# Kernel tuning notes

Measured on AMD Instinct MI355X. Metric: run time of the kernel, lower is better.

## Reference

```python
import jax, jax.numpy as jnp
import numpy as np

N_NODES = 50000
N_EDGES = 800000
NUM_FEATURES = 128
HIDDEN = 128
NUM_GRAPHS = 500


def setup_inputs() -> dict:
    key = jax.random.key(0)
    ks = jax.random.split(key, 8)
    def lin_w(k, fan_in, fan_out):
        bound = 1.0 / np.sqrt(fan_in)
        return jax.random.uniform(k, (fan_in, fan_out), jnp.float32, -bound, bound)
    x = jax.random.normal(ks[0], (N_NODES, NUM_FEATURES), jnp.float32)
    W0 = lin_w(ks[1], NUM_FEATURES, HIDDEN)
    W1 = lin_w(ks[2], HIDDEN, HIDDEN)
    W2 = lin_w(ks[3], HIDDEN, HIDDEN)
    Wout = lin_w(ks[4], HIDDEN, 1)
    b0 = jnp.zeros((HIDDEN,), jnp.float32)
    b1 = jnp.zeros((HIDDEN,), jnp.float32)
    b2 = jnp.zeros((HIDDEN,), jnp.float32)
    bout = jnp.zeros((1,), jnp.float32)
    edge_index = jax.random.randint(ks[5], (2, N_EDGES), 0, N_NODES, jnp.int64)
    batch = jnp.sort(jax.random.randint(ks[6], (N_NODES,), 0, NUM_GRAPHS, jnp.int64))
    return {"x": x, "W0": W0, "b0": b0, "W1": W1, "b1": b1, "W2": W2,
            "b2": b2, "Wout": Wout, "bout": bout,
            "edge_index": edge_index, "batch": batch}


def _gcn_conv(x, W, b, row, col, norm, n_nodes):
    # GCNConv: out = D^{-1/2} (A + I) D^{-1/2} X W + b
    xw = x @ W                                  # [N, H] dense GEMM
    msg = xw[row] * norm[:, None]               # gather + scale  [E+N, H]
    out = jax.ops.segment_sum(msg, col, num_segments=n_nodes)  # scatter-add
    return out + b


def _gcn_norm(edge_index, n_nodes):
    # add self-loops, then symmetric degree normalization
    loops = jnp.arange(n_nodes, dtype=edge_index.dtype)
    row = jnp.concatenate([edge_index[0], loops])  # source (j)
    col = jnp.concatenate([edge_index[1], loops])  # target (i)
    deg = jax.ops.segment_sum(jnp.ones_like(col, dtype=jnp.float32), col,
                              num_segments=n_nodes)
    dinv = jnp.where(deg > 0, jax.lax.rsqrt(jnp.maximum(deg, 1.0)), 0.0)
    norm = dinv[row] * dinv[col]
    return row, col, norm


def reference(x, W0, b0, W1, b1, W2, b2, Wout, bout, edge_index, batch):
    n_nodes = x.shape[0]
    row, col, norm = _gcn_norm(edge_index, n_nodes)
    h = x
    for (W, b) in ((W0, b0), (W1, b1), (W2, b2)):
        h = _gcn_conv(h, W, b, row, col, norm, n_nodes)
        h = jax.nn.elu(h)
        # F.dropout(training=False) -> identity in eval mode
    # global_mean_pool over graph ids
    sums = jax.ops.segment_sum(h, batch, num_segments=NUM_GRAPHS)
    cnts = jax.ops.segment_sum(jnp.ones((n_nodes,), h.dtype), batch,
                               num_segments=NUM_GRAPHS)
    pooled = sums / jnp.maximum(cnts, 1.0)[:, None]   # [G, H]
    return pooled @ Wout + bout                       # [G, 1]
```

## Files before the change

kernel.cpp:

```cpp
#include <hip/hip_runtime.h>
#include <math.h>

#define NN 50000
#define NE 800000
#define HD 128
#define NG 500
#define CAP 48
#define GEMM_BLKS 782
#define FILL_BLKS 384
#define FRONT_GRID (GEMM_BLKS + FILL_BLKS)

__global__ __launch_bounds__(256) void k_front(const float* __restrict__ x,
                                               const float* __restrict__ W,
                                               const int* __restrict__ erow,
                                               const int* __restrict__ ecol,
                                               int* __restrict__ deg,
                                               unsigned short* __restrict__ rec,
                                               float* __restrict__ XW) {
    __shared__ float Hs[64][36];
    __shared__ float Ws[32][132];

    const int bid = blockIdx.x;
    const int tid = threadIdx.x;

    if (bid >= GEMM_BLKS) {
        for (int e = (bid - GEMM_BLKS) * 256 + tid; e < NE; e += FILL_BLKS * 256) {
            int r = erow[e];
            int c = ecol[e];
            int p = atomicAdd(&deg[c], 1);
            p = p < CAP - 1 ? p : CAP - 1;
            rec[c * CAP + p] = (unsigned short)r;
        }
        return;
    }

    const int base = bid * 64;
    const int tr = tid >> 4;
    const int tc = tid & 15;
    const int c0 = tc * 8;

    float acc[4][8];
#pragma unroll
    for (int i = 0; i < 4; ++i)
#pragma unroll
        for (int j = 0; j < 8; ++j) acc[i][j] = 0.f;

    for (int kc = 0; kc < 4; ++kc) {
        __syncthreads();
#pragma unroll
        for (int i = 0; i < 2; ++i) {
            int idx = i * 256 + tid;
            int r = idx >> 3;
            int c4 = idx & 7;
            int row = base + r;
            float4 v = make_float4(0.f, 0.f, 0.f, 0.f);
            if (row < NN) v = *(const float4*)(x + (size_t)row * HD + kc * 32 + c4 * 4);
            *(float4*)&Hs[r][c4 * 4] = v;
        }
#pragma unroll
        for (int i = 0; i < 4; ++i) {
            int idx = i * 256 + tid;
            int kr = idx >> 5;
            int c4 = idx & 31;
            float4 v = *(const float4*)(W + (size_t)(kc * 32 + kr) * HD + c4 * 4);
            *(float4*)&Ws[kr][c4 * 4] = v;
        }
        __syncthreads();
#pragma unroll
        for (int k4 = 0; k4 < 8; ++k4) {
            float ha[4][4];
#pragma unroll
            for (int i = 0; i < 4; ++i) {
                float4 hv = *(const float4*)&Hs[tr + 16 * i][k4 * 4];
                ha[i][0] = hv.x; ha[i][1] = hv.y; ha[i][2] = hv.z; ha[i][3] = hv.w;
            }
#pragma unroll
            for (int q = 0; q < 4; ++q) {
                float4 w0 = *(const float4*)&Ws[k4 * 4 + q][c0];
                float4 w1 = *(const float4*)&Ws[k4 * 4 + q][c0 + 4];
                float wa[8] = {w0.x, w0.y, w0.z, w0.w, w1.x, w1.y, w1.z, w1.w};
#pragma unroll
                for (int i = 0; i < 4; ++i) {
                    float hv = ha[i][q];
#pragma unroll
                    for (int j = 0; j < 8; ++j) acc[i][j] += hv * wa[j];
                }
            }
        }
    }

#pragma unroll
    for (int i = 0; i < 4; ++i) {
        int row = base + tr + 16 * i;
        if (row >= NN) continue;
        float4 x0 = make_float4(acc[i][0], acc[i][1], acc[i][2], acc[i][3]);
        float4 x1 = make_float4(acc[i][4], acc[i][5], acc[i][6], acc[i][7]);
        *(float4*)(XW + (size_t)row * HD + c0)     = x0;
        *(float4*)(XW + (size_t)row * HD + c0 + 4) = x1;
    }
}

__global__ __launch_bounds__(256) void k_prep_scale(const int* __restrict__ deg,
                                                    float* __restrict__ dinv,
                                                    const int* __restrict__ batch,
                                                    int* __restrict__ gptr,
                                                    float* __restrict__ A) {
    __shared__ float sdinv[64];
    const int bid = blockIdx.x;
    const int tid = threadIdx.x;

    if (tid < 64) {
        int row = bid * 64 + tid;
        float d = 0.f;
        if (row < NN) {
            d = rsqrtf((float)(deg[row] + 1));
            dinv[row] = d;
        }
        sdinv[tid] = d;
    }
    int flat = bid * 256 + tid;
    if (flat <= NG) {
        int lo = 0, hi = NN;
        while (lo < hi) {
            int mid = (lo + hi) >> 1;
            if (batch[mid] < flat) lo = mid + 1; else hi = mid;
        }
        gptr[flat] = lo;
    }
    __syncthreads();

#pragma unroll
    for (int i = 0; i < 8; ++i) {
        int idx = i * 256 + tid;
        int r = idx >> 5;
        int c4 = idx & 31;
        int row = bid * 64 + r;
        if (row < NN) {
            float d = sdinv[r];
            float4 v = *(const float4*)(A + (size_t)row * HD + c4 * 4);
            v.x *= d; v.y *= d; v.z *= d; v.w *= d;
            *(float4*)(A + (size_t)row * HD + c4 * 4) = v;
        }
    }
}

__global__ __launch_bounds__(256) void k_gemm(const float* __restrict__ Hin,
                                              const float* __restrict__ W,
                                              float* __restrict__ XW) {
    __shared__ float Hs[64][36];
    __shared__ float Ws[32][132];

    const int tid = threadIdx.x;
    const int base = blockIdx.x * 64;
    const int tr = tid >> 4;
    const int tc = tid & 15;
    const int c0 = tc * 8;

    float acc[4][8];
#pragma unroll
    for (int i = 0; i < 4; ++i)
#pragma unroll
        for (int j = 0; j < 8; ++j) acc[i][j] = 0.f;

    for (int kc = 0; kc < 4; ++kc) {
        __syncthreads();
#pragma unroll
        for (int i = 0; i < 2; ++i) {
            int idx = i * 256 + tid;
            int r = idx >> 3;
            int c4 = idx & 7;
            int row = base + r;
            float4 v = make_float4(0.f, 0.f, 0.f, 0.f);
            if (row < NN) v = *(const float4*)(Hin + (size_t)row * HD + kc * 32 + c4 * 4);
            *(float4*)&Hs[r][c4 * 4] = v;
        }
#pragma unroll
        for (int i = 0; i < 4; ++i) {
            int idx = i * 256 + tid;
            int kr = idx >> 5;
            int c4 = idx & 31;
            float4 v = *(const float4*)(W + (size_t)(kc * 32 + kr) * HD + c4 * 4);
            *(float4*)&Ws[kr][c4 * 4] = v;
        }
        __syncthreads();
#pragma unroll
        for (int k4 = 0; k4 < 8; ++k4) {
            float ha[4][4];
#pragma unroll
            for (int i = 0; i < 4; ++i) {
                float4 hv = *(const float4*)&Hs[tr + 16 * i][k4 * 4];
                ha[i][0] = hv.x; ha[i][1] = hv.y; ha[i][2] = hv.z; ha[i][3] = hv.w;
            }
#pragma unroll
            for (int q = 0; q < 4; ++q) {
                float4 w0 = *(const float4*)&Ws[k4 * 4 + q][c0];
                float4 w1 = *(const float4*)&Ws[k4 * 4 + q][c0 + 4];
                float wa[8] = {w0.x, w0.y, w0.z, w0.w, w1.x, w1.y, w1.z, w1.w};
#pragma unroll
                for (int i = 0; i < 4; ++i) {
                    float hv = ha[i][q];
#pragma unroll
                    for (int j = 0; j < 8; ++j) acc[i][j] += hv * wa[j];
                }
            }
        }
    }

#pragma unroll
    for (int i = 0; i < 4; ++i) {
        int row = base + tr + 16 * i;
        if (row >= NN) continue;
        float4 x0 = make_float4(acc[i][0], acc[i][1], acc[i][2], acc[i][3]);
        float4 x1 = make_float4(acc[i][4], acc[i][5], acc[i][6], acc[i][7]);
        *(float4*)(XW + (size_t)row * HD + c0)     = x0;
        *(float4*)(XW + (size_t)row * HD + c0 + 4) = x1;
    }
}

__device__ __forceinline__ float2 gather_acc(const float* __restrict__ XW,
                                             const unsigned short* __restrict__ rec,
                                             int bb, int deg, int lane) {
    float2 acc = make_float2(0.f, 0.f);
    for (int j = 0; j < deg; j += 8) {
        int src[8];
        float sc[8];
#pragma unroll
        for (int k = 0; k < 8; ++k) {
            int jj = j + k;
            bool ok = jj < deg;
            src[k] = rec[bb + (ok ? jj : 0)];
            sc[k] = ok ? 1.f : 0.f;
        }
        float2 v[8];
#pragma unroll
        for (int k = 0; k < 8; ++k)
            v[k] = ((const float2*)(XW + (size_t)src[k] * HD))[lane];
#pragma unroll
        for (int k = 0; k < 8; ++k) {
            acc.x += v[k].x * sc[k];
            acc.y += v[k].y * sc[k];
        }
    }
    return acc;
}

__global__ __launch_bounds__(256) void k_gather(const float* __restrict__ XW,
                                                float* __restrict__ B,
                                                const unsigned short* __restrict__ rec,
                                                const int* __restrict__ deg,
                                                const float* __restrict__ dinv,
                                                const float* __restrict__ bias) {
    int node = blockIdx.x * 4 + (threadIdx.x >> 6);
    int lane = threadIdx.x & 63;
    if (node >= NN) return;
    float2 acc = gather_acc(XW, rec, node * CAP, deg[node], lane);
    float d = dinv[node];
    float2 xi = ((const float2*)(XW + (size_t)node * HD))[lane];
    float2 bb = ((const float2*)bias)[lane];
    float2 h;
    h.x = d * (acc.x + xi.x) + bb.x;
    h.y = d * (acc.y + xi.y) + bb.y;
    h.x = h.x > 0.f ? h.x : expm1f(h.x);
    h.y = h.y > 0.f ? h.y : expm1f(h.y);
    h.x *= d;
    h.y *= d;
    ((float2*)(B + (size_t)node * HD))[lane] = h;
}

__global__ __launch_bounds__(256) void k_gather_pool(const float* __restrict__ XW,
                                                     const unsigned short* __restrict__ rec,
                                                     const int* __restrict__ deg,
                                                     const float* __restrict__ dinv,
                                                     const float* __restrict__ bias,
                                                     const float* __restrict__ Wout,
                                                     float* __restrict__ nodedot) {
    int node = blockIdx.x * 4 + (threadIdx.x >> 6);
    int lane = threadIdx.x & 63;
    if (node >= NN) return;
    float2 acc = gather_acc(XW, rec, node * CAP, deg[node], lane);
    float d = dinv[node];
    float2 xi = ((const float2*)(XW + (size_t)node * HD))[lane];
    float2 bb = ((const float2*)bias)[lane];
    float2 h;
    h.x = d * (acc.x + xi.x) + bb.x;
    h.y = d * (acc.y + xi.y) + bb.y;
    h.x = h.x > 0.f ? h.x : expm1f(h.x);
    h.y = h.y > 0.f ? h.y : expm1f(h.y);
    float2 w = ((const float2*)Wout)[lane];
    float v = h.x * w.x + h.y * w.y;
#pragma unroll
    for (int off = 32; off > 0; off >>= 1) v += __shfl_down(v, off);
    if (lane == 0) nodedot[node] = v;
}

__global__ __launch_bounds__(64) void k_pool2(const float* __restrict__ nodedot,
                                              const int* __restrict__ gptr,
                                              const float* __restrict__ bout,
                                              float* __restrict__ out) {
    int g = blockIdx.x;
    int lane = threadIdx.x;
    int s = gptr[g];
    int e = gptr[g + 1];
    float acc = 0.f;
    for (int i = s + lane; i < e; i += 64) acc += nodedot[i];
#pragma unroll
    for (int off = 32; off > 0; off >>= 1) acc += __shfl_down(acc, off);
    if (lane == 0) {
        int c = e - s;
        out[g] = acc / (float)(c > 0 ? c : 1) + bout[0];
    }
}

extern "C" void kernel_launch(void* const* d_in, const int* in_sizes, int n_in,
                              void* d_out, int out_size, void* d_ws, size_t ws_size,
                              hipStream_t stream) {
    const float* x    = (const float*)d_in[0];
    const float* W0   = (const float*)d_in[1];
    const float* b0   = (const float*)d_in[2];
    const float* W1   = (const float*)d_in[3];
    const float* b1   = (const float*)d_in[4];
    const float* W2   = (const float*)d_in[5];
    const float* b2   = (const float*)d_in[6];
    const float* Wout = (const float*)d_in[7];
    const float* bout = (const float*)d_in[8];
    const int*   erow = (const int*)d_in[9];
    const int*   ecol = erow + NE;
    const int*   batch = (const int*)d_in[10];
    float* out = (float*)d_out;

    float* A       = (float*)d_ws;
    float* B       = A + (size_t)NN * HD;
    float* dinv    = B + (size_t)NN * HD;
    int*   deg     = (int*)(dinv + NN);
    float* nodedot = (float*)(deg + NN);
    int*   gptr    = (int*)(nodedot + NN);
    unsigned short* rec = (unsigned short*)(gptr + NG + 1);

    hipMemsetAsync(deg, 0, NN * sizeof(int), stream);
    k_front<<<FRONT_GRID, 256, 0, stream>>>(x, W0, erow, ecol, deg, rec, A);
    k_prep_scale<<<GEMM_BLKS, 256, 0, stream>>>(deg, dinv, batch, gptr, A);

    k_gather<<<(NN + 3) / 4, 256, 0, stream>>>(A, B, rec, deg, dinv, b0);
    k_gemm<<<(NN + 63) / 64, 256, 0, stream>>>(B, W1, A);
    k_gather<<<(NN + 3) / 4, 256, 0, stream>>>(A, B, rec, deg, dinv, b1);
    k_gemm<<<(NN + 63) / 64, 256, 0, stream>>>(B, W2, A);
    k_gather_pool<<<(NN + 3) / 4, 256, 0, stream>>>(A, rec, deg, dinv, b2,
                                                    Wout, nodedot);
    k_pool2<<<NG, 64, 0, stream>>>(nodedot, gptr, bout, out);
}
```

Before: 298.6 us.

## Fuse neighbor gather and next-layer GEMM into one kernel per layer

Replaces the separate gather and GEMM kernels for layers 1 and 2 with a single kernel. Each 64-node block first aggregates neighbor features into a shared-memory tile, then multiplies that tile by the next weight matrix. This avoids writing and re-reading the intermediate activation through global memory and removes two launches. In exchange, shared memory per block grows to about 50 KB, which lowers occupancy, and each wave gathers 16 nodes one after another, so the latency hiding the gather kernel had may be lost.

After: 366.7 us. 1.23x slower.

```diff
diff --git a/kernel.cpp b/kernel.cpp
--- a/kernel.cpp
+++ b/kernel.cpp
@@ -144,79 +144,6 @@
     }
 }
 
-__global__ __launch_bounds__(256) void k_gemm(const float* __restrict__ Hin,
-                                              const float* __restrict__ W,
-                                              float* __restrict__ XW) {
-    __shared__ float Hs[64][36];
-    __shared__ float Ws[32][132];
-
-    const int tid = threadIdx.x;
-    const int base = blockIdx.x * 64;
-    const int tr = tid >> 4;
-    const int tc = tid & 15;
-    const int c0 = tc * 8;
-
-    float acc[4][8];
-#pragma unroll
-    for (int i = 0; i < 4; ++i)
-#pragma unroll
-        for (int j = 0; j < 8; ++j) acc[i][j] = 0.f;
-
-    for (int kc = 0; kc < 4; ++kc) {
-        __syncthreads();
-#pragma unroll
-        for (int i = 0; i < 2; ++i) {
-            int idx = i * 256 + tid;
-            int r = idx >> 3;
-            int c4 = idx & 7;
-            int row = base + r;
-            float4 v = make_float4(0.f, 0.f, 0.f, 0.f);
-            if (row < NN) v = *(const float4*)(Hin + (size_t)row * HD + kc * 32 + c4 * 4);
-            *(float4*)&Hs[r][c4 * 4] = v;
-        }
-#pragma unroll
-        for (int i = 0; i < 4; ++i) {
-            int idx = i * 256 + tid;
-            int kr = idx >> 5;
-            int c4 = idx & 31;
-            float4 v = *(const float4*)(W + (size_t)(kc * 32 + kr) * HD + c4 * 4);
-            *(float4*)&Ws[kr][c4 * 4] = v;
-        }
-        __syncthreads();
-#pragma unroll
-        for (int k4 = 0; k4 < 8; ++k4) {
-            float ha[4][4];
-#pragma unroll
-            for (int i = 0; i < 4; ++i) {
-                float4 hv = *(const float4*)&Hs[tr + 16 * i][k4 * 4];
-                ha[i][0] = hv.x; ha[i][1] = hv.y; ha[i][2] = hv.z; ha[i][3] = hv.w;
-            }
-#pragma unroll
-            for (int q = 0; q < 4; ++q) {
-                float4 w0 = *(const float4*)&Ws[k4 * 4 + q][c0];
-                float4 w1 = *(const float4*)&Ws[k4 * 4 + q][c0 + 4];
-                float wa[8] = {w0.x, w0.y, w0.z, w0.w, w1.x, w1.y, w1.z, w1.w};
-#pragma unroll
-                for (int i = 0; i < 4; ++i) {
-                    float hv = ha[i][q];
-#pragma unroll
-                    for (int j = 0; j < 8; ++j) acc[i][j] += hv * wa[j];
-                }
-            }
-        }
-    }
-
-#pragma unroll
-    for (int i = 0; i < 4; ++i) {
-        int row = base + tr + 16 * i;
-        if (row >= NN) continue;
-        float4 x0 = make_float4(acc[i][0], acc[i][1], acc[i][2], acc[i][3]);
-        float4 x1 = make_float4(acc[i][4], acc[i][5], acc[i][6], acc[i][7]);
-        *(float4*)(XW + (size_t)row * HD + c0)     = x0;
-        *(float4*)(XW + (size_t)row * HD + c0 + 4) = x1;
-    }
-}
-
 __device__ __forceinline__ float2 gather_acc(const float* __restrict__ XW,
                                              const unsigned short* __restrict__ rec,
                                              int bb, int deg, int lane) {
@@ -244,27 +171,92 @@
     return acc;
 }
 
-__global__ __launch_bounds__(256) void k_gather(const float* __restrict__ XW,
-                                                float* __restrict__ B,
-                                                const unsigned short* __restrict__ rec,
-                                                const int* __restrict__ deg,
-                                                const float* __restrict__ dinv,
-                                                const float* __restrict__ bias) {
-    int node = blockIdx.x * 4 + (threadIdx.x >> 6);
-    int lane = threadIdx.x & 63;
-    if (node >= NN) return;
-    float2 acc = gather_acc(XW, rec, node * CAP, deg[node], lane);
-    float d = dinv[node];
-    float2 xi = ((const float2*)(XW + (size_t)node * HD))[lane];
-    float2 bb = ((const float2*)bias)[lane];
-    float2 h;
-    h.x = d * (acc.x + xi.x) + bb.x;
-    h.y = d * (acc.y + xi.y) + bb.y;
-    h.x = h.x > 0.f ? h.x : expm1f(h.x);
-    h.y = h.y > 0.f ? h.y : expm1f(h.y);
-    h.x *= d;
-    h.y *= d;
-    ((float2*)(B + (size_t)node * HD))[lane] = h;
+__global__ __launch_bounds__(256) void k_fused(const float* __restrict__ Ain,
+                                               const float* __restrict__ W,
+                                               const unsigned short* __restrict__ rec,
+                                               const int* __restrict__ deg,
+                                               const float* __restrict__ dinv,
+                                               const float* __restrict__ bias,
+                                               float* __restrict__ Aout) {
+    __shared__ float Ht[64][132];
+    __shared__ float Ws[32][132];
+
+    const int tid = threadIdx.x;
+    const int base = blockIdx.x * 64;
+    const int wv = tid >> 6;
+    const int lane = tid & 63;
+
+    const float2 bb = ((const float2*)bias)[lane];
+    for (int n = wv * 16; n < wv * 16 + 16; ++n) {
+        int node = base + n;
+        float2 h = make_float2(0.f, 0.f);
+        if (node < NN) {
+            float2 acc = gather_acc(Ain, rec, node * CAP, deg[node], lane);
+            float d = dinv[node];
+            float2 xi = ((const float2*)(Ain + (size_t)node * HD))[lane];
+            h.x = d * (acc.x + xi.x) + bb.x;
+            h.y = d * (acc.y + xi.y) + bb.y;
+            h.x = h.x > 0.f ? h.x : expm1f(h.x);
+            h.y = h.y > 0.f ? h.y : expm1f(h.y);
+            h.x *= d;
+            h.y *= d;
+        }
+        *(float2*)&Ht[n][lane * 2] = h;
+    }
+
+    const int tr = tid >> 4;
+    const int tc = tid & 15;
+    const int c0 = tc * 8;
+
+    float acc[4][8];
+#pragma unroll
+    for (int i = 0; i < 4; ++i)
+#pragma unroll
+        for (int j = 0; j < 8; ++j) acc[i][j] = 0.f;
+
+    for (int kc = 0; kc < 4; ++kc) {
+        __syncthreads();
+#pragma unroll
+        for (int i = 0; i < 4; ++i) {
+            int idx = i * 256 + tid;
+            int kr = idx >> 5;
+            int c4 = idx & 31;
+            float4 v = *(const float4*)(W + (size_t)(kc * 32 + kr) * HD + c4 * 4);
+            *(float4*)&Ws[kr][c4 * 4] = v;
+        }
+        __syncthreads();
+#pragma unroll
+        for (int k4 = 0; k4 < 8; ++k4) {
+            float ha[4][4];
+#pragma unroll
+            for (int i = 0; i < 4; ++i) {
+                float4 hv = *(const float4*)&Ht[tr + 16 * i][kc * 32 + k4 * 4];
+                ha[i][0] = hv.x; ha[i][1] = hv.y; ha[i][2] = hv.z; ha[i][3] = hv.w;
+            }
+#pragma unroll
+            for (int q = 0; q < 4; ++q) {
+                float4 w0 = *(const float4*)&Ws[k4 * 4 + q][c0];
+                float4 w1 = *(const float4*)&Ws[k4 * 4 + q][c0 + 4];
+                float wa[8] = {w0.x, w0.y, w0.z, w0.w, w1.x, w1.y, w1.z, w1.w};
+#pragma unroll
+                for (int i = 0; i < 4; ++i) {
+                    float hv = ha[i][q];
+#pragma unroll
+                    for (int j = 0; j < 8; ++j) acc[i][j] += hv * wa[j];
+                }
+            }
+        }
+    }
+
+#pragma unroll
+    for (int i = 0; i < 4; ++i) {
+        int row = base + tr + 16 * i;
+        if (row >= NN) continue;
+        float4 x0 = make_float4(acc[i][0], acc[i][1], acc[i][2], acc[i][3]);
+        float4 x1 = make_float4(acc[i][4], acc[i][5], acc[i][6], acc[i][7]);
+        *(float4*)(Aout + (size_t)row * HD + c0)     = x0;
+        *(float4*)(Aout + (size_t)row * HD + c0 + 4) = x1;
+    }
 }
 
 __global__ __launch_bounds__(256) void k_gather_pool(const float* __restrict__ XW,
@@ -340,10 +332,8 @@
     k_front<<<FRONT_GRID, 256, 0, stream>>>(x, W0, erow, ecol, deg, rec, A);
     k_prep_scale<<<GEMM_BLKS, 256, 0, stream>>>(deg, dinv, batch, gptr, A);
 
-    k_gather<<<(NN + 3) / 4, 256, 0, stream>>>(A, B, rec, deg, dinv, b0);
-    k_gemm<<<(NN + 63) / 64, 256, 0, stream>>>(B, W1, A);
-    k_gather<<<(NN + 3) / 4, 256, 0, stream>>>(A, B, rec, deg, dinv, b1);
-    k_gemm<<<(NN + 63) / 64, 256, 0, stream>>>(B, W2, A);
+    k_fused<<<GEMM_BLKS, 256, 0, stream>>>(A, W1, rec, deg, dinv, b0, B);
+    k_fused<<<GEMM_BLKS, 256, 0, stream>>>(B, W2, rec, deg, dinv, b1, A);
     k_gather_pool<<<(NN + 3) / 4, 256, 0, stream>>>(A, rec, deg, dinv, b2,
                                                     Wout, nodedot);
     k_pool2<<<NG, 64, 0, stream>>>(nodedot, gptr, bout, out);
```
